# Kernel optimization log

Hardware: AMD Instinct MI355X
Metric: run time of the kernel (lower is better)

## Reference

```python
import jax, jax.numpy as jnp
import numpy as np

N_NODES = 50000
N_EDGES = 800000
IN_CH = 128
HID = 128


def _linear_params(key, fan_in, fan_out):
    kw, kb = jax.random.split(key)
    bound = 1.0 / np.sqrt(fan_in)
    W = jax.random.uniform(kw, (fan_in, fan_out), jnp.float32, -bound, bound)
    b = jax.random.uniform(kb, (fan_out,), jnp.float32, -bound, bound)
    return W, b


def setup_inputs() -> dict:
    key = jax.random.key(0)
    ks = jax.random.split(key, 11)
    x = jax.random.normal(ks[0], (N_NODES, IN_CH), jnp.float32)
    guidance_features = jax.random.normal(ks[1], (N_NODES, HID), jnp.float32)
    edge_index = jax.random.randint(ks[2], (2, N_EDGES), 0, N_NODES, jnp.int64)
    node_W, node_b = _linear_params(ks[3], IN_CH, HID)
    nbr_W, nbr_b = _linear_params(ks[4], IN_CH, HID)
    gud_W, gud_b = _linear_params(ks[5], HID, HID)
    enc_W, enc_b = _linear_params(ks[6], 3 * HID, HID)
    vp_W1, vp_b1 = _linear_params(ks[7], HID, HID // 2)
    vp_W2, vp_b2 = _linear_params(ks[8], HID // 2, 1)
    pol_W1, pol_b1 = _linear_params(ks[9], HID, HID)
    pol_W2, pol_b2 = _linear_params(ks[10], HID, 1)
    return dict(x=x, edge_index=edge_index, guidance_features=guidance_features,
                node_W=node_W, node_b=node_b, nbr_W=nbr_W, nbr_b=nbr_b,
                gud_W=gud_W, gud_b=gud_b, enc_W=enc_W, enc_b=enc_b,
                vp_W1=vp_W1, vp_b1=vp_b1, vp_W2=vp_W2, vp_b2=vp_b2,
                pol_W1=pol_W1, pol_b1=pol_b1, pol_W2=pol_W2, pol_b2=pol_b2)


def reference(x, edge_index, guidance_features,
              node_W, node_b, nbr_W, nbr_b, gud_W, gud_b,
              enc_W, enc_b, vp_W1, vp_b1, vp_W2, vp_b2,
              pol_W1, pol_b1, pol_W2, pol_b2):
    row, col = edge_index[0], edge_index[1]
    # Edge-wise gathers feeding three linear transforms -> [E, 3*HID] state
    node_feat = x[row] @ node_W + node_b            # [E, HID]
    nbr_feat = x[col] @ nbr_W + nbr_b               # [E, HID]
    gud_feat = guidance_features[col] @ gud_W + gud_b  # [E, HID]
    state = jnp.concatenate([node_feat, nbr_feat, gud_feat], axis=1)
    # state_encoder (eval mode: dropout = identity)
    enc = jax.nn.relu(state @ enc_W + enc_b)        # [E, HID]
    # value_predictor
    value_preds = jax.nn.relu(enc @ vp_W1 + vp_b1) @ vp_W2 + vp_b2  # [E, 1]
    # policy_net
    action_probs = jax.nn.sigmoid(
        jax.nn.relu(enc @ pol_W1 + pol_b1) @ pol_W2 + pol_b2)      # [E, 1]
    actions = (action_probs > 0.5).astype(x.dtype)  # eval-mode actions
    value_loss = jnp.zeros((), x.dtype)             # eval mode, labels=None
    return value_preds, action_probs, actions, value_loss
```

## Files before the change

### kernel.cpp

```cpp
#include <hip/hip_runtime.h>
#include <math.h>

#define N_NODES 50000
#define N_EDGES 800000

typedef __attribute__((ext_vector_type(8))) short short8_t;
typedef __attribute__((ext_vector_type(4))) float float4_t;

union U8 { short8_t v; unsigned short u[8]; };

__device__ __forceinline__ unsigned short bf16_rn(float f) {
    unsigned u = __float_as_uint(f);
    u += 0x7fffu + ((u >> 16) & 1u);
    return (unsigned short)(u >> 16);
}
__device__ __forceinline__ float bf2f(unsigned short h) {
    return __uint_as_float((unsigned)h << 16);
}
__device__ __forceinline__ void split3(float f, unsigned short& s0,
                                       unsigned short& s1, unsigned short& s2) {
    s0 = bf16_rn(f);  float r = f - bf2f(s0);
    s1 = bf16_rn(r);  r -= bf2f(s1);
    s2 = bf16_rn(r);
}
__device__ __forceinline__ void split3t(float f, unsigned short& s0,
                                        unsigned short& s1, unsigned short& s2) {
    unsigned u = __float_as_uint(f);
    s0 = (unsigned short)(u >> 16);
    float r = f - bf2f(s0);
    unsigned v = __float_as_uint(r);
    s1 = (unsigned short)(v >> 16);
    float r2 = r - bf2f(s1);
    s2 = bf16_rn(r2);
}


__global__ __launch_bounds__(256) void prep_kernel(
    const float* __restrict__ node_W, const float* __restrict__ node_b,
    const float* __restrict__ nbr_W,  const float* __restrict__ nbr_b,
    const float* __restrict__ gud_W,  const float* __restrict__ gud_b,
    const float* __restrict__ enc_W,  const float* __restrict__ enc_b,
    const float* __restrict__ vp_W1,  const float* __restrict__ vp_b1,
    const float* __restrict__ vp_W2,  const float* __restrict__ pol_W1,
    const float* __restrict__ pol_b1, const float* __restrict__ pol_W2,
    unsigned short* __restrict__ BTn0, unsigned short* __restrict__ BTn1,
    unsigned short* __restrict__ BTn2,
    unsigned short* __restrict__ BTg0, unsigned short* __restrict__ BTg1,
    unsigned short* __restrict__ BTg2,
    unsigned short* __restrict__ BTw0, unsigned short* __restrict__ BTw1,
    unsigned short* __restrict__ BTw2,
    float* __restrict__ cb, float* __restrict__ b1c, float* __restrict__ W2c,
    int* __restrict__ flags)
{
    const int k = blockIdx.x;
    const int j = threadIdx.x;
    if (j < 128) {
        float a = 0.f, b = 0.f;
        #pragma unroll 4
        for (int m = 0; m < 128; ++m) {
            a = fmaf(node_W[k * 128 + m], enc_W[m * 128 + j], a);
            b = fmaf(gud_W [k * 128 + m], enc_W[(256 + m) * 128 + j], b);
        }
        size_t i1 = (size_t)j * 128 + k;
        split3(a, BTn0[i1], BTn1[i1], BTn2[i1]);
        split3(b, BTg0[i1], BTg1[i1], BTg2[i1]);
    } else {
        const int n = j - 128;
        float a = 0.f;
        #pragma unroll 4
        for (int m = 0; m < 128; ++m)
            a = fmaf(nbr_W[k * 128 + m], enc_W[(128 + m) * 128 + n], a);
        size_t i2 = (size_t)(128 + n) * 128 + k;
        split3(a, BTn0[i2], BTn1[i2], BTn2[i2]);
    }
    if (j < 192) {
        float wv = (j < 64) ? vp_W1[k * 64 + j] : pol_W1[k * 128 + (j - 64)];
        size_t iw = (size_t)j * 128 + k;
        split3(wv, BTw0[iw], BTw1[iw], BTw2[iw]);
    }
    if (k == 0) {
        if (j < 128) {
            float cc = enc_b[j];
            for (int m = 0; m < 128; ++m) {
                cc = fmaf(node_b[m], enc_W[m * 128 + j], cc);
                cc = fmaf(nbr_b [m], enc_W[(128 + m) * 128 + j], cc);
                cc = fmaf(gud_b [m], enc_W[(256 + m) * 128 + j], cc);
            }
            cb[j] = cc;
        }
        if (j < 192) {
            b1c[j] = (j < 64) ? vp_b1[j] : pol_b1[j - 64];
            W2c[j] = (j < 64) ? vp_W2[j] : pol_W2[j - 64];
        }
        if (j < 64) {
            const int l = j, li = l & 15, lq = l >> 4;
            U8 A, B;
            #pragma unroll
            for (int u = 0; u < 8; ++u) { A.u[u] = 0; B.u[u] = 0; }
            if (lq == 0) {
                A.u[0] = bf16_rn((float)(li + 1));
                A.u[1] = bf16_rn(1.0f);
                B.u[0] = bf16_rn(1.0f);
                B.u[1] = bf16_rn((float)(100 * (li + 1)));
            }
            float4_t d = (float4_t){0.f, 0.f, 0.f, 0.f};
            d = __builtin_amdgcn_mfma_f32_16x16x32_bf16(A.v, B.v, d, 0, 0, 0);
            if (l == 17) {
                flags[0] = (fabsf(d[2] - 702.f) < 1.0f) ? 1 : 0;
            }
        }
    }
}

__global__ __launch_bounds__(256, 3) void node_kernel(
    const float* __restrict__ x, const float* __restrict__ g,
    const unsigned short* __restrict__ BTn0, const unsigned short* __restrict__ BTn1,
    const unsigned short* __restrict__ BTn2,
    const unsigned short* __restrict__ BTg0, const unsigned short* __restrict__ BTg1,
    const unsigned short* __restrict__ BTg2,
    const float* __restrict__ cb, const int* __restrict__ flags,
    float* __restrict__ P, float* __restrict__ Q)
{
    __shared__ unsigned short a0s[4 * 64 * 8];
    __shared__ unsigned short a1s[4 * 64 * 8];
    __shared__ unsigned short a2s[4 * 64 * 8];
    const int t = threadIdx.x;
    const int w = t >> 6, lane = t & 63;
    const int i16 = lane & 15, q = lane >> 4;
    const int base = blockIdx.x * 64;
    const int swap = flags[0];
    const int el = t >> 2, hh = t & 3;
    int nodeL = base + el; if (nodeL > N_NODES - 1) nodeL = N_NODES - 1;
    const float* xrow = x + (size_t)nodeL * 128 + hh * 8;
    const float* grow = g + (size_t)nodeL * 128 + hh * 8;

    float4_t acc[4][4];
    #pragma unroll
    for (int mt = 0; mt < 4; ++mt)
        #pragma unroll
        for (int nt = 0; nt < 4; ++nt) acc[mt][nt] = (float4_t){0.f, 0.f, 0.f, 0.f};

    float4 pv0 = *(const float4*)(xrow);
    float4 pv1 = *(const float4*)(xrow + 4);

    for (int kc = 0; kc < 8; ++kc) {
        U8 s0, s1, s2;
        {
            float e[8] = {pv0.x, pv0.y, pv0.z, pv0.w, pv1.x, pv1.y, pv1.z, pv1.w};
            #pragma unroll
            for (int u = 0; u < 8; ++u) split3t(e[u], s0.u[u], s1.u[u], s2.u[u]);
        }
        __syncthreads();
        {
            size_t off = ((size_t)hh * 64 + el) * 8;
            *(short8_t*)(a0s + off) = s0.v;
            *(short8_t*)(a1s + off) = s1.v;
            *(short8_t*)(a2s + off) = s2.v;
        }
        __syncthreads();
        if (kc < 7) {
            const float* nsrc = (kc + 1 < 4) ? (xrow + (kc + 1) * 32)
                                             : (grow + (kc + 1 - 4) * 32);
            pv0 = *(const float4*)(nsrc);
            pv1 = *(const float4*)(nsrc + 4);
        }
        if (kc < 4) {
            short8_t b0[4], b1v[4], b2v[4];
            #pragma unroll
            for (int ntl = 0; ntl < 4; ++ntl) {
                int ntg = w + ntl * 4;
                size_t roff = ((size_t)(ntg * 16 + i16)) * 128 + kc * 32 + q * 8;
                b0[ntl]  = *(const short8_t*)(BTn0 + roff);
                b1v[ntl] = *(const short8_t*)(BTn1 + roff);
                b2v[ntl] = *(const short8_t*)(BTn2 + roff);
            }
            #pragma unroll
            for (int mt = 0; mt < 4; ++mt) {
                size_t aoff = ((size_t)q * 64 + mt * 16 + i16) * 8;
                short8_t a0 = *(const short8_t*)(a0s + aoff);
                short8_t a1 = *(const short8_t*)(a1s + aoff);
                short8_t a2 = *(const short8_t*)(a2s + aoff);
                #pragma unroll
                for (int ntl = 0; ntl < 4; ++ntl) {
                    float4_t c = acc[mt][ntl];
                    c = __builtin_amdgcn_mfma_f32_16x16x32_bf16(a0, b0[ntl],  c, 0, 0, 0);
                    c = __builtin_amdgcn_mfma_f32_16x16x32_bf16(a0, b1v[ntl], c, 0, 0, 0);
                    c = __builtin_amdgcn_mfma_f32_16x16x32_bf16(a1, b0[ntl],  c, 0, 0, 0);
                    c = __builtin_amdgcn_mfma_f32_16x16x32_bf16(a0, b2v[ntl], c, 0, 0, 0);
                    c = __builtin_amdgcn_mfma_f32_16x16x32_bf16(a1, b1v[ntl], c, 0, 0, 0);
                    c = __builtin_amdgcn_mfma_f32_16x16x32_bf16(a2, b0[ntl],  c, 0, 0, 0);
                    acc[mt][ntl] = c;
                }
            }
        } else {
            short8_t b0[2], b1v[2], b2v[2];
            #pragma unroll
            for (int ntl = 0; ntl < 2; ++ntl) {
                int ntg = w + (ntl + 2) * 4;
                size_t roff = ((size_t)((ntg - 8) * 16 + i16)) * 128 + (kc - 4) * 32 + q * 8;
                b0[ntl]  = *(const short8_t*)(BTg0 + roff);
                b1v[ntl] = *(const short8_t*)(BTg1 + roff);
                b2v[ntl] = *(const short8_t*)(BTg2 + roff);
            }
            #pragma unroll
            for (int mt = 0; mt < 4; ++mt) {
                size_t aoff = ((size_t)q * 64 + mt * 16 + i16) * 8;
                short8_t a0 = *(const short8_t*)(a0s + aoff);
                short8_t a1 = *(const short8_t*)(a1s + aoff);
                short8_t a2 = *(const short8_t*)(a2s + aoff);
                #pragma unroll
                for (int ntl = 0; ntl < 2; ++ntl) {
                    float4_t c = acc[mt][ntl + 2];
                    c = __builtin_amdgcn_mfma_f32_16x16x32_bf16(a0, b0[ntl],  c, 0, 0, 0);
                    c = __builtin_amdgcn_mfma_f32_16x16x32_bf16(a0, b1v[ntl], c, 0, 0, 0);
                    c = __builtin_amdgcn_mfma_f32_16x16x32_bf16(a1, b0[ntl],  c, 0, 0, 0);
                    c = __builtin_amdgcn_mfma_f32_16x16x32_bf16(a0, b2v[ntl], c, 0, 0, 0);
                    c = __builtin_amdgcn_mfma_f32_16x16x32_bf16(a1, b1v[ntl], c, 0, 0, 0);
                    c = __builtin_amdgcn_mfma_f32_16x16x32_bf16(a2, b0[ntl],  c, 0, 0, 0);
                    acc[mt][ntl + 2] = c;
                }
            }
        }
    }

    if (!swap) {
        #pragma unroll
        for (int mt = 0; mt < 4; ++mt)
            #pragma unroll
            for (int ntl = 0; ntl < 4; ++ntl) {
                int ntg = w + ntl * 4;
                int chan = ntg * 16 + i16;
                bool isP = (ntg < 8);
                float bias = isP ? cb[chan] : 0.f;
                #pragma unroll
                for (int r = 0; r < 4; ++r) {
                    int node = base + mt * 16 + q * 4 + r;
                    if (node < N_NODES) {
                        if (isP) P[(size_t)node * 128 + chan] = acc[mt][ntl][r] + bias;
                        else     Q[(size_t)node * 128 + (chan - 128)] = acc[mt][ntl][r];
                    }
                }
            }
    } else {
        #pragma unroll
        for (int mt = 0; mt < 4; ++mt) {
            int node = base + mt * 16 + i16;
            if (node < N_NODES) {
                #pragma unroll
                for (int ntl = 0; ntl < 4; ++ntl) {
                    int ntg = w + ntl * 4;
                    int chanb = ntg * 16 + q * 4;
                    bool isP = (ntg < 8);
                    float4 vv;
                    vv.x = acc[mt][ntl][0] + (isP ? cb[chanb + 0] : 0.f);
                    vv.y = acc[mt][ntl][1] + (isP ? cb[chanb + 1] : 0.f);
                    vv.z = acc[mt][ntl][2] + (isP ? cb[chanb + 2] : 0.f);
                    vv.w = acc[mt][ntl][3] + (isP ? cb[chanb + 3] : 0.f);
                    if (isP) *(float4*)(P + (size_t)node * 128 + chanb) = vv;
                    else     *(float4*)(Q + (size_t)node * 128 + chanb - 128) = vv;
                }
            }
        }
    }
}

__global__ __launch_bounds__(256, 2) void edge_kernel(
    const int* __restrict__ ei,
    const float* __restrict__ P, const float* __restrict__ Q,
    const unsigned short* __restrict__ BTw0, const unsigned short* __restrict__ BTw1,
    const unsigned short* __restrict__ BTw2,
    const float* __restrict__ b1c, const float* __restrict__ W2c,
    const float* __restrict__ vp_b2, const float* __restrict__ pol_b2,
    const int* __restrict__ flags,
    float* __restrict__ out)
{
    __shared__ unsigned short enc0[4 * 128 * 8];
    __shared__ unsigned short enc1[4 * 128 * 8];
    __shared__ unsigned short enc2[4 * 128 * 8];
    __shared__ float vpart[512], ppart[512];

    const int t = threadIdx.x;
    const int w = t >> 6, lane = t & 63;
    const int i16 = lane & 15, q = lane >> 4;
    const int e0 = blockIdx.x * 128;
    const int ntg0 = w * 3;
    const int el = t >> 1, hh = t & 1;
    const int swap = flags[0];

    const int rowI = ei[e0 + el];
    const int colI = ei[N_EDGES + e0 + el];
    const float* Pp = P + (size_t)rowI * 128 + hh * 16;
    const float* Qp = Q + (size_t)colI * 128 + hh * 16;

    float4_t acc[8][3];
    #pragma unroll
    for (int mt = 0; mt < 8; ++mt)
        #pragma unroll
        for (int nt = 0; nt < 3; ++nt) acc[mt][nt] = (float4_t){0.f, 0.f, 0.f, 0.f};

    float4 pv[4], qv[4];
    #pragma unroll
    for (int i = 0; i < 4; ++i) {
        pv[i] = *(const float4*)(Pp + i * 4);
        qv[i] = *(const float4*)(Qp + i * 4);
    }

    for (int kc = 0; kc < 4; ++kc) {
        U8 g0[2], g1[2], g2[2];
        #pragma unroll
        for (int i = 0; i < 4; ++i) {
            float ev[4] = {fmaxf(pv[i].x + qv[i].x, 0.f), fmaxf(pv[i].y + qv[i].y, 0.f),
                           fmaxf(pv[i].z + qv[i].z, 0.f), fmaxf(pv[i].w + qv[i].w, 0.f)};
            #pragma unroll
            for (int u = 0; u < 4; ++u) {
                int idx = i * 4 + u;
                split3t(ev[u], g0[idx >> 3].u[idx & 7], g1[idx >> 3].u[idx & 7],
                        g2[idx >> 3].u[idx & 7]);
            }
        }
        __syncthreads();
        #pragma unroll
        for (int hb = 0; hb < 2; ++hb) {
            size_t off = ((size_t)(2 * hh + hb) * 128 + el) * 8;
            *(short8_t*)(enc0 + off) = g0[hb].v;
            *(short8_t*)(enc1 + off) = g1[hb].v;
            *(short8_t*)(enc2 + off) = g2[hb].v;
        }
        __syncthreads();
        if (kc < 3) {
            #pragma unroll
            for (int i = 0; i < 4; ++i) {
                pv[i] = *(const float4*)(Pp + (kc + 1) * 32 + i * 4);
                qv[i] = *(const float4*)(Qp + (kc + 1) * 32 + i * 4);
            }
        }
        short8_t b0[3], b1f[3], b2f[3];
        #pragma unroll
        for (int ntl = 0; ntl < 3; ++ntl) {
            size_t roff = ((size_t)((ntg0 + ntl) * 16 + i16)) * 128 + kc * 32 + q * 8;
            b0[ntl]  = *(const short8_t*)(BTw0 + roff);
            b1f[ntl] = *(const short8_t*)(BTw1 + roff);
            b2f[ntl] = *(const short8_t*)(BTw2 + roff);
        }
        #pragma unroll
        for (int mt = 0; mt < 8; ++mt) {
            size_t aoff = ((size_t)q * 128 + mt * 16 + i16) * 8;
            short8_t a0 = *(const short8_t*)(enc0 + aoff);
            short8_t a1 = *(const short8_t*)(enc1 + aoff);
            short8_t a2 = *(const short8_t*)(enc2 + aoff);
            #pragma unroll
            for (int ntl = 0; ntl < 3; ++ntl) {
                float4_t c = acc[mt][ntl];
                c = __builtin_amdgcn_mfma_f32_16x16x32_bf16(a0, b0[ntl],  c, 0, 0, 0);
                c = __builtin_amdgcn_mfma_f32_16x16x32_bf16(a0, b1f[ntl], c, 0, 0, 0);
                c = __builtin_amdgcn_mfma_f32_16x16x32_bf16(a1, b0[ntl],  c, 0, 0, 0);
                c = __builtin_amdgcn_mfma_f32_16x16x32_bf16(a0, b2f[ntl], c, 0, 0, 0);
                c = __builtin_amdgcn_mfma_f32_16x16x32_bf16(a1, b1f[ntl], c, 0, 0, 0);
                c = __builtin_amdgcn_mfma_f32_16x16x32_bf16(a2, b0[ntl],  c, 0, 0, 0);
                acc[mt][ntl] = c;
            }
        }
    }

    if (!swap) {
        #pragma unroll
        for (int mt = 0; mt < 8; ++mt) {
            float vs[4] = {0.f, 0.f, 0.f, 0.f}, ps[4] = {0.f, 0.f, 0.f, 0.f};
            #pragma unroll
            for (int ntl = 0; ntl < 3; ++ntl) {
                int ntg = ntg0 + ntl;
                int n = ntg * 16 + i16;
                float b1s = b1c[n], w2s = W2c[n];
                bool isv = (ntg < 4);
                #pragma unroll
                for (int r = 0; r < 4; ++r) {
                    float hv = fmaxf(acc[mt][ntl][r] + b1s, 0.f) * w2s;
                    if (isv) vs[r] += hv; else ps[r] += hv;
                }
            }
            #pragma unroll
            for (int off = 1; off < 16; off <<= 1)
                #pragma unroll
                for (int r = 0; r < 4; ++r) {
                    vs[r] += __shfl_xor(vs[r], off, 64);
                    ps[r] += __shfl_xor(ps[r], off, 64);
                }
            if (i16 == 0)
                #pragma unroll
                for (int r = 0; r < 4; ++r) {
                    int eidx = mt * 16 + q * 4 + r;
                    vpart[w * 128 + eidx] = vs[r];
                    ppart[w * 128 + eidx] = ps[r];
                }
        }
    } else {
        #pragma unroll
        for (int mt = 0; mt < 8; ++mt) {
            float v = 0.f, p = 0.f;
            #pragma unroll
            for (int ntl = 0; ntl < 3; ++ntl) {
                int ntg = ntg0 + ntl;
                bool isv = (ntg < 4);
                #pragma unroll
                for (int r = 0; r < 4; ++r) {
                    int n = ntg * 16 + q * 4 + r;
                    float hv = fmaxf(acc[mt][ntl][r] + b1c[n], 0.f) * W2c[n];
                    if (isv) v += hv; else p += hv;
                }
            }
            v += __shfl_xor(v, 16, 64); v += __shfl_xor(v, 32, 64);
            p += __shfl_xor(p, 16, 64); p += __shfl_xor(p, 32, 64);
            if (q == 0) {
                int eidx = mt * 16 + i16;
                vpart[w * 128 + eidx] = v;
                ppart[w * 128 + eidx] = p;
            }
        }
    }
    __syncthreads();
    if (t < 128) {
        float v  = vpart[t] + vpart[128 + t] + vpart[256 + t] + vpart[384 + t] + vp_b2[0];
        float pl = ppart[t] + ppart[128 + t] + ppart[256 + t] + ppart[384 + t] + pol_b2[0];
        float prob = 1.0f / (1.0f + expf(-pl));
        int e = e0 + t;
        out[e] = v;
        out[N_EDGES + e] = prob;
        out[2 * N_EDGES + e] = (prob > 0.5f) ? 1.0f : 0.0f;
    }
    if (blockIdx.x == 0 && t == 0) out[3 * N_EDGES] = 0.0f;
}

extern "C" void kernel_launch(void* const* d_in, const int* in_sizes, int n_in,
                              void* d_out, int out_size, void* d_ws, size_t ws_size,
                              hipStream_t stream) {
    const float* x      = (const float*)d_in[0];
    const int*   ei     = (const int*)  d_in[1];
    const float* gf     = (const float*)d_in[2];
    const float* node_W = (const float*)d_in[3];
    const float* node_b = (const float*)d_in[4];
    const float* nbr_W  = (const float*)d_in[5];
    const float* nbr_b  = (const float*)d_in[6];
    const float* gud_W  = (const float*)d_in[7];
    const float* gud_b  = (const float*)d_in[8];
    const float* enc_W  = (const float*)d_in[9];
    const float* enc_b  = (const float*)d_in[10];
    const float* vp_W1  = (const float*)d_in[11];
    const float* vp_b1  = (const float*)d_in[12];
    const float* vp_W2  = (const float*)d_in[13];
    const float* vp_b2  = (const float*)d_in[14];
    const float* pol_W1 = (const float*)d_in[15];
    const float* pol_b1 = (const float*)d_in[16];
    const float* pol_W2 = (const float*)d_in[17];
    const float* pol_b2 = (const float*)d_in[18];
    float* out = (float*)d_out;

    unsigned char* wsb = (unsigned char*)d_ws;
    unsigned short* BTn0 = (unsigned short*)(wsb + 0);
    unsigned short* BTn1 = (unsigned short*)(wsb + 65536);
    unsigned short* BTn2 = (unsigned short*)(wsb + 131072);
    unsigned short* BTg0 = (unsigned short*)(wsb + 196608);
    unsigned short* BTg1 = (unsigned short*)(wsb + 229376);
    unsigned short* BTg2 = (unsigned short*)(wsb + 262144);
    unsigned short* BTw0 = (unsigned short*)(wsb + 294912);
    unsigned short* BTw1 = (unsigned short*)(wsb + 344064);
    unsigned short* BTw2 = (unsigned short*)(wsb + 393216);
    float* cb   = (float*)(wsb + 442368);
    float* b1c  = (float*)(wsb + 442880);
    float* W2c  = (float*)(wsb + 443648);
    int*   flags= (int*)  (wsb + 444416);
    float* Pd   = (float*)(wsb + 444480);
    float* Qd   = Pd + (size_t)N_NODES * 128;

    prep_kernel<<<dim3(128), dim3(256), 0, stream>>>(
        node_W, node_b, nbr_W, nbr_b, gud_W, gud_b, enc_W, enc_b,
        vp_W1, vp_b1, vp_W2, pol_W1, pol_b1, pol_W2,
        BTn0, BTn1, BTn2, BTg0, BTg1, BTg2, BTw0, BTw1, BTw2,
        cb, b1c, W2c, flags);

    node_kernel<<<dim3((N_NODES + 63) / 64), dim3(256), 0, stream>>>(
        x, gf, BTn0, BTn1, BTn2, BTg0, BTg1, BTg2, cb, flags, Pd, Qd);

    edge_kernel<<<dim3(N_EDGES / 128), dim3(256), 0, stream>>>(
        ei, Pd, Qd, BTw0, BTw1, BTw2, b1c, W2c, vp_b2, pol_b2, flags, out);
}
```

Baseline: 518.9 us.

## Double-buffer edge-kernel LDS tiles and prefetch next weight fragments

The LDS staging buffers for the split-bf16 activations are doubled and alternated across k-chunks, which removes one __syncthreads per iteration. The weight fragments for the next k-chunk are loaded from global memory before the current chunk's MFMAs, so that load latency overlaps with compute. The cost is twice the LDS footprint and extra vector registers for the prefetched fragments. Under launch_bounds(256,2) this could cause register spills or lower occupancy.

Measured after the change: 524.7 us. Within noise of the previous version (+1.1%).

```diff
diff --git a/kernel.cpp b/kernel.cpp
--- a/kernel.cpp
+++ b/kernel.cpp
@@ -274,9 +274,9 @@
     const int* __restrict__ flags,
     float* __restrict__ out)
 {
-    __shared__ unsigned short enc0[4 * 128 * 8];
-    __shared__ unsigned short enc1[4 * 128 * 8];
-    __shared__ unsigned short enc2[4 * 128 * 8];
+    __shared__ unsigned short enc0[2][4 * 128 * 8];
+    __shared__ unsigned short enc1[2][4 * 128 * 8];
+    __shared__ unsigned short enc2[2][4 * 128 * 8];
     __shared__ float vpart[512], ppart[512];
 
     const int t = threadIdx.x;
@@ -304,8 +304,18 @@
         pv[i] = *(const float4*)(Pp + i * 4);
         qv[i] = *(const float4*)(Qp + i * 4);
     }
-
+    short8_t b0[3], b1f[3], b2f[3];
+    #pragma unroll
+    for (int ntl = 0; ntl < 3; ++ntl) {
+        size_t roff = ((size_t)((ntg0 + ntl) * 16 + i16)) * 128 + q * 8;
+        b0[ntl]  = *(const short8_t*)(BTw0 + roff);
+        b1f[ntl] = *(const short8_t*)(BTw1 + roff);
+        b2f[ntl] = *(const short8_t*)(BTw2 + roff);
+    }
+
+    #pragma unroll
     for (int kc = 0; kc < 4; ++kc) {
+        const int kb = kc & 1;
         U8 g0[2], g1[2], g2[2];
         #pragma unroll
         for (int i = 0; i < 4; ++i) {
@@ -318,13 +328,12 @@
                         g2[idx >> 3].u[idx & 7]);
             }
         }
-        __syncthreads();
         #pragma unroll
         for (int hb = 0; hb < 2; ++hb) {
             size_t off = ((size_t)(2 * hh + hb) * 128 + el) * 8;
-            *(short8_t*)(enc0 + off) = g0[hb].v;
-            *(short8_t*)(enc1 + off) = g1[hb].v;
-            *(short8_t*)(enc2 + off) = g2[hb].v;
+            *(short8_t*)(enc0[kb] + off) = g0[hb].v;
+            *(short8_t*)(enc1[kb] + off) = g1[hb].v;
+            *(short8_t*)(enc2[kb] + off) = g2[hb].v;
         }
         __syncthreads();
         if (kc < 3) {
@@ -334,20 +343,22 @@
                 qv[i] = *(const float4*)(Qp + (kc + 1) * 32 + i * 4);
             }
         }
-        short8_t b0[3], b1f[3], b2f[3];
-        #pragma unroll
-        for (int ntl = 0; ntl < 3; ++ntl) {
-            size_t roff = ((size_t)((ntg0 + ntl) * 16 + i16)) * 128 + kc * 32 + q * 8;
-            b0[ntl]  = *(const short8_t*)(BTw0 + roff);
-            b1f[ntl] = *(const short8_t*)(BTw1 + roff);
-            b2f[ntl] = *(const short8_t*)(BTw2 + roff);
+        short8_t nb0[3], nb1[3], nb2[3];
+        if (kc < 3) {
+            #pragma unroll
+            for (int ntl = 0; ntl < 3; ++ntl) {
+                size_t roff = ((size_t)((ntg0 + ntl) * 16 + i16)) * 128 + (kc + 1) * 32 + q * 8;
+                nb0[ntl] = *(const short8_t*)(BTw0 + roff);
+                nb1[ntl] = *(const short8_t*)(BTw1 + roff);
+                nb2[ntl] = *(const short8_t*)(BTw2 + roff);
+            }
         }
         #pragma unroll
         for (int mt = 0; mt < 8; ++mt) {
             size_t aoff = ((size_t)q * 128 + mt * 16 + i16) * 8;
-            short8_t a0 = *(const short8_t*)(enc0 + aoff);
-            short8_t a1 = *(const short8_t*)(enc1 + aoff);
-            short8_t a2 = *(const short8_t*)(enc2 + aoff);
+            short8_t a0 = *(const short8_t*)(enc0[kb] + aoff);
+            short8_t a1 = *(const short8_t*)(enc1[kb] + aoff);
+            short8_t a2 = *(const short8_t*)(enc2[kb] + aoff);
             #pragma unroll
             for (int ntl = 0; ntl < 3; ++ntl) {
                 float4_t c = acc[mt][ntl];
@@ -358,6 +369,12 @@
                 c = __builtin_amdgcn_mfma_f32_16x16x32_bf16(a1, b1f[ntl], c, 0, 0, 0);
                 c = __builtin_amdgcn_mfma_f32_16x16x32_bf16(a2, b0[ntl],  c, 0, 0, 0);
                 acc[mt][ntl] = c;
+            }
+        }
+        if (kc < 3) {
+            #pragma unroll
+            for (int ntl = 0; ntl < 3; ++ntl) {
+                b0[ntl] = nb0[ntl]; b1f[ntl] = nb1[ntl]; b2f[ntl] = nb2[ntl];
             }
         }
     }
```
